# Optimization experiments

Measured on AMD Instinct MI355X. Metric: run time of the kernel, lower is better.

The kernel has to match this reference:

```python
import jax, jax.numpy as jnp
import numpy as np
from jax import lax

RATE = 0.3  # drop_rate from init_kwargs
B, L, E, U, V = 32, 64, 512, 512, 32000


def setup_inputs() -> dict:
    key = jax.random.key(0)
    ks = jax.random.split(key, 9)
    return {
        "pos_embs": jax.random.normal(ks[0], (B, L, E), jnp.float32),
        "images_emb": jax.random.normal(ks[1], (B, E), jnp.float32),
        "targets": jax.random.randint(ks[2], (B, L), 0, V, jnp.int64),
        # learned parameters
        "emb_table": jax.random.normal(ks[3], (V, E), jnp.float32) * 0.02,
        "W_in": jax.random.normal(ks[4], (E, 4 * U), jnp.float32) * 0.05,   # LSTM kernel (gate order i,f,c,o)
        "W_rec": jax.random.normal(ks[5], (U, 4 * U), jnp.float32) * 0.05,  # LSTM recurrent kernel
        "b_lstm": jnp.zeros((4 * U,), jnp.float32),
        "W_out": jax.random.normal(ks[6], (U, V), jnp.float32) * 0.02,
        "b_out": jnp.zeros((V,), jnp.float32),
    }


def _dropout_masks(batch, seq_len):
    """Deterministic dropout masks (training=True in the original)."""
    keep = 1.0 - RATE
    mk = jax.random.key(42)
    k1, k2, k3 = jax.random.split(mk, 3)
    # word dropout: noise_shape=(None,1,E) -> one mask per (batch, feature), shared over time
    word_mask = jax.random.bernoulli(k1, keep, (batch, 1, E)).astype(jnp.float32) / keep
    # Keras recurrent_dropout: 4 masks on h (one per gate), constant across timesteps
    rec_masks = jax.random.bernoulli(k2, keep, (4, batch, U)).astype(jnp.float32) / keep
    # final dropout on rnn_output [B, T, units]
    fin_mask = jax.random.bernoulli(k3, keep, (batch, seq_len, U)).astype(jnp.float32) / keep
    return word_mask, rec_masks, fin_mask


def reference(pos_embs, images_emb, targets, emb_table, W_in, W_rec, b_lstm, W_out, b_out):
    batch = pos_embs.shape[0]
    seq_len = targets.shape[1]  # (L-1) words + 1 image step = L
    word_mask, rec_masks, fin_mask = _dropout_masks(batch, seq_len)

    # embedding + word dropout (mask shared over time axis)
    word_embs = emb_table[targets[:, :-1]] * word_mask            # [B, L-1, E]
    x = jnp.concatenate([images_emb[:, None, :], word_embs], axis=1)  # [B, L, E]

    W_rec_g = W_rec.reshape(U, 4, U)  # [u, gate, u]

    def step(carry, x_t):
        h, c = carry
        z_in = x_t @ W_in + b_lstm                                # [B, 4U]
        # per-gate recurrent dropout on h, then recurrent matmul
        z_rec = jnp.einsum('gbu,ugv->bgv', h[None, :, :] * rec_masks, W_rec_g)
        z = z_in + z_rec.reshape(batch, 4 * U)
        zi, zf, zg, zo = jnp.split(z, 4, axis=-1)
        i = jax.nn.sigmoid(zi)
        f = jax.nn.sigmoid(zf)
        g = jnp.tanh(zg)
        o = jax.nn.sigmoid(zo)
        c_new = f * c + i * g
        h_new = o * jnp.tanh(c_new)
        return (h_new, c_new), h_new

    h0 = jnp.zeros((batch, U), x.dtype)
    (_, _), hs = lax.scan(step, (h0, h0), x.transpose(1, 0, 2))   # hs: [L, B, U]
    rnn_out = hs.transpose(1, 0, 2) * fin_mask                    # [B, L, U]

    predictions = rnn_out @ W_out + b_out                         # [B, L, V]
    return predictions
```

## Files before the change

### kernel.cpp

```cpp
#include <hip/hip_runtime.h>
#include <hip/hip_bf16.h>
#include <cstdint>
#include <cstddef>

struct TF2 { uint32_t a, b; };

__host__ __device__ constexpr uint32_t rotl32(uint32_t v, int r) {
  return (v << r) | (v >> (32 - r));
}

__host__ __device__ constexpr TF2 threefry2x32(uint32_t k0, uint32_t k1,
                                               uint32_t x0, uint32_t x1) {
  uint32_t ks0 = k0, ks1 = k1, ks2 = k0 ^ k1 ^ 0x1BD11BDAu;
  const int rotA[4] = {13, 15, 26, 6};
  const int rotB[4] = {17, 29, 16, 24};
  x0 += ks0; x1 += ks1;
  for (int i = 0; i < 5; ++i) {
    const int* rot = (i % 2 == 0) ? rotA : rotB;
    for (int j = 0; j < 4; ++j) {
      x0 += x1; x1 = rotl32(x1, rot[j]); x1 ^= x0;
    }
    uint32_t ks[3] = {ks0, ks1, ks2};
    x0 += ks[(i + 1) % 3];
    x1 += ks[(i + 2) % 3] + (uint32_t)(i + 1);
  }
  return TF2{x0, x1};
}

__device__ __forceinline__ float jax_mask(uint32_t child, uint32_t idx) {
  TF2 ck = threefry2x32(0u, 42u, 0u, child);
  TF2 r  = threefry2x32(ck.a, ck.b, 0u, idx);
  uint32_t bits = r.a ^ r.b;
  float u = __uint_as_float((bits >> 9) | 0x3f800000u) - 1.0f;
  return (u < 0.7f) ? (1.0f / 0.7f) : 0.0f;
}

__device__ __forceinline__ unsigned short f2bf(float f) {
  uint32_t u = __float_as_uint(f);
  uint32_t r = (u + 0x7fffu + ((u >> 16) & 1u)) >> 16;
  return (unsigned short)r;
}

typedef __attribute__((ext_vector_type(8))) short short8;
typedef __attribute__((ext_vector_type(4))) float f32x4;

__device__ __forceinline__ void async_copy16(const unsigned short* g, unsigned short* l) {
  __builtin_amdgcn_global_load_lds(
      (const __attribute__((address_space(1))) unsigned int*)g,
      (__attribute__((address_space(3))) unsigned int*)l, 16, 0, 0);
}

__global__ __launch_bounds__(256) void build_x_kernel(
    const float* __restrict__ img, const int* __restrict__ tgt,
    const float* __restrict__ emb, unsigned short* __restrict__ x) {
  const int idx = blockIdx.x * 256 + threadIdx.x;
  const int e = idx & 511;
  const int t = (idx >> 9) & 63;
  const int b = idx >> 15;
  float v;
  if (t == 0) {
    v = img[b * 512 + e];
  } else {
    const int w = tgt[b * 64 + (t - 1)];
    const float wm = jax_mask(0u, (uint32_t)(b * 512 + e));
    v = emb[(size_t)w * 512 + e] * wm;
  }
  x[idx] = f2bf(v);
}

__global__ __launch_bounds__(256) void rec_mask_kernel(float* __restrict__ rm) {
  const int idx = blockIdx.x * 256 + threadIdx.x;
  rm[idx] = jax_mask(1u, (uint32_t)idx);
}

__global__ __launch_bounds__(256) void transpose_wrec(
    const float* __restrict__ in, float* __restrict__ out) {
  __shared__ float tile[32][33];
  const int j0 = blockIdx.x * 32;
  const int u0 = blockIdx.y * 32;
  const int tx = threadIdx.x & 31;
  const int ty = threadIdx.x >> 5;
  for (int r = ty; r < 32; r += 8)
    tile[r][tx] = in[(size_t)(u0 + r) * 2048 + (j0 + tx)];
  __syncthreads();
  for (int r = ty; r < 32; r += 8)
    out[(size_t)(j0 + r) * 512 + (u0 + tx)] = tile[tx][r];
}

__global__ __launch_bounds__(256) void transpose_cvt(
    const float* __restrict__ in, unsigned short* __restrict__ out,
    int R, int C) {
  __shared__ float tile[32][33];
  const int c0 = blockIdx.x * 32;
  const int r0 = blockIdx.y * 32;
  const int tx = threadIdx.x & 31;
  const int ty = threadIdx.x >> 5;
  for (int r = ty; r < 32; r += 8)
    tile[r][tx] = in[(size_t)(r0 + r) * C + (c0 + tx)];
  __syncthreads();
  for (int r = ty; r < 32; r += 8)
    out[(size_t)(c0 + r) * R + (r0 + tx)] = f2bf(tile[tx][r]);
}

__global__ __launch_bounds__(256) void gemm_bf16_mfma(
    const unsigned short* __restrict__ A, const unsigned short* __restrict__ BT,
    const float* __restrict__ bias, float* __restrict__ C, int M, int N) {
  __shared__ unsigned short As[128 * 32];
  __shared__ unsigned short Bs[128 * 32];
  const int tid = threadIdx.x;
  const int lane = tid & 63;
  const int wave = tid >> 6;
  const int wm = (wave >> 1) * 64;
  const int wn = (wave & 1) * 64;
  const int m0 = blockIdx.y * 128;
  const int n0 = blockIdx.x * 128;

  f32x4 zero4 = {0.f, 0.f, 0.f, 0.f};
  f32x4 acc[4][4];
#pragma unroll
  for (int i = 0; i < 4; ++i)
#pragma unroll
    for (int j = 0; j < 4; ++j) acc[i][j] = zero4;

  const unsigned short* ga = A + (size_t)(m0 + (tid >> 2)) * 512 + (tid & 3) * 8;
  const unsigned short* gb = BT + (size_t)(n0 + (tid >> 2)) * 512 + (tid & 3) * 8;
  unsigned short* lwA = As + wave * 512;
  unsigned short* lwB = Bs + wave * 512;

  const int fr = lane & 15;
  const int kc = (lane >> 4) * 8;

  for (int k0 = 0; k0 < 512; k0 += 32) {
    __syncthreads();
    async_copy16(ga + k0, lwA);
    async_copy16(ga + k0 + 64 * 512, lwA + 2048);
    async_copy16(gb + k0, lwB);
    async_copy16(gb + k0 + 64 * 512, lwB + 2048);
    __syncthreads();

    short8 af[4], bf[4];
#pragma unroll
    for (int i = 0; i < 4; ++i)
      af[i] = *(const short8*)(As + (wm + i * 16 + fr) * 32 + kc);
#pragma unroll
    for (int i = 0; i < 4; ++i)
      bf[i] = *(const short8*)(Bs + (wn + i * 16 + fr) * 32 + kc);
#pragma unroll
    for (int mi = 0; mi < 4; ++mi)
#pragma unroll
      for (int ni = 0; ni < 4; ++ni)
        acc[mi][ni] = __builtin_amdgcn_mfma_f32_16x16x32_bf16(
            af[mi], bf[ni], acc[mi][ni], 0, 0, 0);
  }

#pragma unroll
  for (int mi = 0; mi < 4; ++mi) {
    const int mrow = m0 + wm + mi * 16 + (lane >> 4) * 4;
#pragma unroll
    for (int ni = 0; ni < 4; ++ni) {
      const int ncol = n0 + wn + ni * 16 + (lane & 15);
      const float bs = bias[ncol];
#pragma unroll
      for (int r2 = 0; r2 < 4; ++r2)
        C[(size_t)(mrow + r2) * N + ncol] = acc[mi][ni][r2] + bs;
    }
  }
}

__global__ __launch_bounds__(256) void lstm_step2(
    const float* __restrict__ zin, const float* __restrict__ WT,
    const float* __restrict__ rm, const float* __restrict__ hmr,
    float* __restrict__ hmw, float* __restrict__ c,
    unsigned short* __restrict__ rnn, const int t) {
  __shared__ __align__(16) float wl[32 * 132];
  __shared__ __align__(16) float hl[32 * 132];
  __shared__ float zsh[4][8][9];
  const int tid = threadIdx.x;
  const int u0 = (blockIdx.x & 63) * 8;
  const int b0 = (blockIdx.x >> 6) * 8;

  const int jl = tid & 31;
  const int bl = tid >> 5;
  const int g = jl >> 3, ul = jl & 7;
  const int b = b0 + bl;
  const float zv = zin[(size_t)(b * 64 + t) * 2048 + g * 512 + u0 + ul];

  const int srow = tid >> 3;
  const int sg = srow >> 3, sr = srow & 7;
  const float* wsrc = WT + (size_t)(sg * 512 + u0 + sr) * 512;
  const float* hsrc = hmr + (size_t)(sg * 32 + b0 + sr) * 512;

  const float4* wp = (const float4*)&wl[jl * 132];
  const float4* hp = (const float4*)&hl[(g * 8 + bl) * 132];

  float4 a0 = {0.f, 0.f, 0.f, 0.f}, a1 = {0.f, 0.f, 0.f, 0.f};

  for (int ph = 0; ph < 4; ++ph) {
    const int kbase = ph * 128;
    __syncthreads();
#pragma unroll
    for (int cc = 0; cc < 4; ++cc) {
      const int ch = (tid & 7) + cc * 8;
      *(float4*)&wl[srow * 132 + ch * 4] = *(const float4*)&wsrc[kbase + ch * 4];
      *(float4*)&hl[srow * 132 + ch * 4] = *(const float4*)&hsrc[kbase + ch * 4];
    }
    __syncthreads();
#pragma unroll 8
    for (int i = 0; i < 32; i += 2) {
      const float4 w0 = wp[i], h0 = hp[i];
      const float4 w1 = wp[i + 1], h1 = hp[i + 1];
      a0.x += w0.x * h0.x; a0.y += w0.y * h0.y;
      a0.z += w0.z * h0.z; a0.w += w0.w * h0.w;
      a1.x += w1.x * h1.x; a1.y += w1.y * h1.y;
      a1.z += w1.z * h1.z; a1.w += w1.w * h1.w;
    }
  }
  const float dot = (a0.x + a0.y + a0.z + a0.w) + (a1.x + a1.y + a1.z + a1.w);
  zsh[g][bl][ul] = zv + dot;
  __syncthreads();

  if (tid < 64) {
    const int uu = tid & 7, bb = tid >> 3;
    const float zi = zsh[0][bb][uu];
    const float zf = zsh[1][bb][uu];
    const float zg = zsh[2][bb][uu];
    const float zo = zsh[3][bb][uu];
    const float i_ = 1.f / (1.f + expf(-zi));
    const float f_ = 1.f / (1.f + expf(-zf));
    const float g_ = tanhf(zg);
    const float o_ = 1.f / (1.f + expf(-zo));
    const int bg = b0 + bb, ug = u0 + uu;
    const size_t cidx = (size_t)bg * 512 + ug;
    const float cn = f_ * c[cidx] + i_ * g_;
    c[cidx] = cn;
    const float hn = o_ * tanhf(cn);
    const float fm = jax_mask(2u, (uint32_t)((bg * 64 + t) * 512 + ug));
    rnn[(size_t)(bg * 64 + t) * 512 + ug] = f2bf(hn * fm);
#pragma unroll
    for (int gg = 0; gg < 4; ++gg) {
      const size_t o = (size_t)(gg * 32 + bg) * 512 + ug;
      hmw[o] = hn * rm[o];
    }
  }
}

extern "C" void kernel_launch(void* const* d_in, const int* in_sizes, int n_in,
                              void* d_out, int out_size, void* d_ws, size_t ws_size,
                              hipStream_t stream) {
  (void)in_sizes; (void)n_in; (void)out_size; (void)ws_size;
  const float* img   = (const float*)d_in[1];
  const int*   tgt   = (const int*)d_in[2];
  const float* emb   = (const float*)d_in[3];
  const float* W_in  = (const float*)d_in[4];
  const float* W_rec = (const float*)d_in[5];
  const float* b_l   = (const float*)d_in[6];
  const float* W_out = (const float*)d_in[7];
  const float* b_o   = (const float*)d_in[8];
  float* out = (float*)d_out;
  float* ws  = (float*)d_ws;

  float* zin = ws;
  float* WT  = ws + 4194304;
  float* hm0 = ws + 5242880;
  float* c   = ws + 5308416;
  float* hm1 = ws + 5324800;
  float* rm  = ws + 5390336;
  unsigned short* us = (unsigned short*)(ws + 5455872);
  unsigned short* x_bf  = us;
  unsigned short* WinT  = us + 1048576;
  unsigned short* rnn   = us + 2097152;
  unsigned short* WoutT = us + 3145728;

  hipMemsetAsync(hm0, 0, (size_t)(65536 + 16384) * sizeof(float), stream);

  build_x_kernel<<<4096, 256, 0, stream>>>(img, tgt, emb, x_bf);
  rec_mask_kernel<<<256, 256, 0, stream>>>(rm);
  transpose_wrec<<<dim3(64, 16), 256, 0, stream>>>(W_rec, WT);
  transpose_cvt<<<dim3(64, 16), 256, 0, stream>>>(W_in, WinT, 512, 2048);
  transpose_cvt<<<dim3(1000, 16), 256, 0, stream>>>(W_out, WoutT, 512, 32000);

  gemm_bf16_mfma<<<dim3(16, 16), 256, 0, stream>>>(x_bf, WinT, b_l, zin, 2048, 2048);

  for (int t = 0; t < 64; ++t) {
    const float* hr = (t & 1) ? hm1 : hm0;
    float*       hw = (t & 1) ? hm0 : hm1;
    lstm_step2<<<256, 256, 0, stream>>>(zin, WT, rm, hr, hw, c, rnn, t);
  }

  gemm_bf16_mfma<<<dim3(250, 16), 256, 0, stream>>>(rnn, WoutT, b_o, out, 2048, 32000);
}
```

Measured before the change: 1.088 ms.

## Replace per-step LSTM launches with persistent kernel using grid barrier and split-bf16 MFMA

Runs the 64 LSTM timesteps inside one persistent 32-block kernel synchronized by an atomic grid barrier, instead of launching one kernel per step. Recurrent weights are kept in registers as hi/lo bf16 pairs and the recurrent matmul uses MFMA with a three-product split to keep near-fp32 accuracy. Recurrent masks and the cell state move into registers. This is meant to remove launch overhead and repeated weight reloads. In exchange it relies on all 32 blocks being co-resident, since the launch is not cooperative, and the split-bf16 products change rounding slightly.

```diff
diff --git a/kernel.cpp b/kernel.cpp
--- a/kernel.cpp
+++ b/kernel.cpp
@@ -39,6 +39,10 @@
   uint32_t u = __float_as_uint(f);
   uint32_t r = (u + 0x7fffu + ((u >> 16) & 1u)) >> 16;
   return (unsigned short)r;
+}
+
+__device__ __forceinline__ float bf2f(unsigned short b) {
+  return __uint_as_float((uint32_t)b << 16);
 }
 
 typedef __attribute__((ext_vector_type(8))) short short8;
@@ -68,11 +72,6 @@
   x[idx] = f2bf(v);
 }
 
-__global__ __launch_bounds__(256) void rec_mask_kernel(float* __restrict__ rm) {
-  const int idx = blockIdx.x * 256 + threadIdx.x;
-  rm[idx] = jax_mask(1u, (uint32_t)idx);
-}
-
 __global__ __launch_bounds__(256) void transpose_wrec(
     const float* __restrict__ in, float* __restrict__ out) {
   __shared__ float tile[32][33];
@@ -167,80 +166,129 @@
   }
 }
 
-__global__ __launch_bounds__(256) void lstm_step2(
+#define HM_PSTRIDE (2 * 4 * 32 * 512)
+#define NBLK 32
+
+__device__ __forceinline__ void grid_barrier(unsigned int* bar, unsigned int target) {
+  __syncthreads();
+  __threadfence();
+  if (threadIdx.x == 0) {
+    __hip_atomic_fetch_add(bar, 1u, __ATOMIC_RELAXED, __HIP_MEMORY_SCOPE_AGENT);
+    while (__hip_atomic_load(bar, __ATOMIC_RELAXED, __HIP_MEMORY_SCOPE_AGENT) < target)
+      __builtin_amdgcn_s_sleep(1);
+  }
+  __syncthreads();
+  __threadfence();
+}
+
+__global__ __launch_bounds__(256, 1) void lstm_coop(
     const float* __restrict__ zin, const float* __restrict__ WT,
-    const float* __restrict__ rm, const float* __restrict__ hmr,
-    float* __restrict__ hmw, float* __restrict__ c,
-    unsigned short* __restrict__ rnn, const int t) {
-  __shared__ __align__(16) float wl[32 * 132];
-  __shared__ __align__(16) float hl[32 * 132];
-  __shared__ float zsh[4][8][9];
+    unsigned short* __restrict__ hm, unsigned short* __restrict__ rnn,
+    unsigned int* __restrict__ bar) {
+  __shared__ float zsh[4][32][17];
   const int tid = threadIdx.x;
-  const int u0 = (blockIdx.x & 63) * 8;
-  const int b0 = (blockIdx.x >> 6) * 8;
-
-  const int jl = tid & 31;
-  const int bl = tid >> 5;
-  const int g = jl >> 3, ul = jl & 7;
-  const int b = b0 + bl;
-  const float zv = zin[(size_t)(b * 64 + t) * 2048 + g * 512 + u0 + ul];
-
-  const int srow = tid >> 3;
-  const int sg = srow >> 3, sr = srow & 7;
-  const float* wsrc = WT + (size_t)(sg * 512 + u0 + sr) * 512;
-  const float* hsrc = hmr + (size_t)(sg * 32 + b0 + sr) * 512;
-
-  const float4* wp = (const float4*)&wl[jl * 132];
-  const float4* hp = (const float4*)&hl[(g * 8 + bl) * 132];
-
-  float4 a0 = {0.f, 0.f, 0.f, 0.f}, a1 = {0.f, 0.f, 0.f, 0.f};
-
-  for (int ph = 0; ph < 4; ++ph) {
-    const int kbase = ph * 128;
+  const int lane = tid & 63;
+  const int g = tid >> 6;
+  const int u0 = blockIdx.x * 16;
+  const int fr = lane & 15;
+  const int kq = (lane >> 4) * 8;
+
+  short8 whi[16], wlo[16];
+  {
+    const float* wrow = WT + (size_t)(g * 512 + u0 + fr) * 512 + kq;
+#pragma unroll
+    for (int kk = 0; kk < 16; ++kk) {
+      const float4 w0 = *(const float4*)(wrow + kk * 32);
+      const float4 w1 = *(const float4*)(wrow + kk * 32 + 4);
+      const float wv[8] = {w0.x, w0.y, w0.z, w0.w, w1.x, w1.y, w1.z, w1.w};
+      short8 h8, l8;
+#pragma unroll
+      for (int e = 0; e < 8; ++e) {
+        const unsigned short hb = f2bf(wv[e]);
+        h8[e] = (short)hb;
+        l8[e] = (short)f2bf(wv[e] - bf2f(hb));
+      }
+      whi[kk] = h8; wlo[kk] = l8;
+    }
+  }
+
+  const int ab = tid >> 4;
+  const int uc = tid & 15;
+  const int au = u0 + uc;
+  float rmask[2][4];
+#pragma unroll
+  for (int cc = 0; cc < 2; ++cc)
+#pragma unroll
+    for (int gg = 0; gg < 4; ++gg)
+      rmask[cc][gg] = jax_mask(1u, (uint32_t)((gg * 32 + ab + cc * 16) * 512 + au));
+  float c0 = 0.f, c1 = 0.f;
+
+  for (int t = 0; t < 64; ++t) {
+    const int rp = t & 1;
+    f32x4 ahh0 = {0,0,0,0}, ahl0 = {0,0,0,0}, alh0 = {0,0,0,0};
+    f32x4 ahh1 = {0,0,0,0}, ahl1 = {0,0,0,0}, alh1 = {0,0,0,0};
+
+    if (t) {
+      const unsigned short* hb  = hm + (size_t)rp * HM_PSTRIDE;
+      const unsigned short* hhi = hb + (size_t)((0 * 4 + g) * 32) * 512;
+      const unsigned short* hlo = hb + (size_t)((1 * 4 + g) * 32) * 512;
+#pragma unroll
+      for (int kk = 0; kk < 16; ++kk) {
+        const int ko = kk * 32 + kq;
+        const short8 ah0 = *(const short8*)(hhi + (size_t)(fr) * 512 + ko);
+        const short8 ah1 = *(const short8*)(hhi + (size_t)(16 + fr) * 512 + ko);
+        const short8 al0 = *(const short8*)(hlo + (size_t)(fr) * 512 + ko);
+        const short8 al1 = *(const short8*)(hlo + (size_t)(16 + fr) * 512 + ko);
+        ahh0 = __builtin_amdgcn_mfma_f32_16x16x32_bf16(ah0, whi[kk], ahh0, 0, 0, 0);
+        ahh1 = __builtin_amdgcn_mfma_f32_16x16x32_bf16(ah1, whi[kk], ahh1, 0, 0, 0);
+        ahl0 = __builtin_amdgcn_mfma_f32_16x16x32_bf16(ah0, wlo[kk], ahl0, 0, 0, 0);
+        ahl1 = __builtin_amdgcn_mfma_f32_16x16x32_bf16(ah1, wlo[kk], ahl1, 0, 0, 0);
+        alh0 = __builtin_amdgcn_mfma_f32_16x16x32_bf16(al0, whi[kk], alh0, 0, 0, 0);
+        alh1 = __builtin_amdgcn_mfma_f32_16x16x32_bf16(al1, whi[kk], alh1, 0, 0, 0);
+      }
+    }
+
+#pragma unroll
+    for (int r = 0; r < 4; ++r) {
+      zsh[g][(lane >> 4) * 4 + r][fr]      = ahh0[r] + ahl0[r] + alh0[r];
+      zsh[g][16 + (lane >> 4) * 4 + r][fr] = ahh1[r] + ahl1[r] + alh1[r];
+    }
     __syncthreads();
-#pragma unroll
-    for (int cc = 0; cc < 4; ++cc) {
-      const int ch = (tid & 7) + cc * 8;
-      *(float4*)&wl[srow * 132 + ch * 4] = *(const float4*)&wsrc[kbase + ch * 4];
-      *(float4*)&hl[srow * 132 + ch * 4] = *(const float4*)&hsrc[kbase + ch * 4];
-    }
-    __syncthreads();
-#pragma unroll 8
-    for (int i = 0; i < 32; i += 2) {
-      const float4 w0 = wp[i], h0 = hp[i];
-      const float4 w1 = wp[i + 1], h1 = hp[i + 1];
-      a0.x += w0.x * h0.x; a0.y += w0.y * h0.y;
-      a0.z += w0.z * h0.z; a0.w += w0.w * h0.w;
-      a1.x += w1.x * h1.x; a1.y += w1.y * h1.y;
-      a1.z += w1.z * h1.z; a1.w += w1.w * h1.w;
-    }
-  }
-  const float dot = (a0.x + a0.y + a0.z + a0.w) + (a1.x + a1.y + a1.z + a1.w);
-  zsh[g][bl][ul] = zv + dot;
-  __syncthreads();
-
-  if (tid < 64) {
-    const int uu = tid & 7, bb = tid >> 3;
-    const float zi = zsh[0][bb][uu];
-    const float zf = zsh[1][bb][uu];
-    const float zg = zsh[2][bb][uu];
-    const float zo = zsh[3][bb][uu];
-    const float i_ = 1.f / (1.f + expf(-zi));
-    const float f_ = 1.f / (1.f + expf(-zf));
-    const float g_ = tanhf(zg);
-    const float o_ = 1.f / (1.f + expf(-zo));
-    const int bg = b0 + bb, ug = u0 + uu;
-    const size_t cidx = (size_t)bg * 512 + ug;
-    const float cn = f_ * c[cidx] + i_ * g_;
-    c[cidx] = cn;
-    const float hn = o_ * tanhf(cn);
-    const float fm = jax_mask(2u, (uint32_t)((bg * 64 + t) * 512 + ug));
-    rnn[(size_t)(bg * 64 + t) * 512 + ug] = f2bf(hn * fm);
-#pragma unroll
-    for (int gg = 0; gg < 4; ++gg) {
-      const size_t o = (size_t)(gg * 32 + bg) * 512 + ug;
-      hmw[o] = hn * rm[o];
-    }
+
+    float hn[2];
+#pragma unroll
+    for (int cc = 0; cc < 2; ++cc) {
+      const int b = ab + cc * 16;
+      const size_t zo = (size_t)(b * 64 + t) * 2048 + au;
+      const float zi = zsh[0][b][uc] + zin[zo];
+      const float zf = zsh[1][b][uc] + zin[zo + 512];
+      const float zg = zsh[2][b][uc] + zin[zo + 1024];
+      const float zz = zsh[3][b][uc] + zin[zo + 1536];
+      const float i_ = 1.f / (1.f + expf(-zi));
+      const float f_ = 1.f / (1.f + expf(-zf));
+      const float g_ = tanhf(zg);
+      const float o_ = 1.f / (1.f + expf(-zz));
+      float& c = cc ? c1 : c0;
+      c = f_ * c + i_ * g_;
+      hn[cc] = o_ * tanhf(c);
+      const float fm = jax_mask(2u, (uint32_t)((b * 64 + t) * 512 + au));
+      rnn[(size_t)(b * 64 + t) * 512 + au] = f2bf(hn[cc] * fm);
+    }
+
+    unsigned short* hw = hm + (size_t)(rp ^ 1) * HM_PSTRIDE;
+#pragma unroll
+    for (int cc = 0; cc < 2; ++cc) {
+      const int b = ab + cc * 16;
+#pragma unroll
+      for (int gg = 0; gg < 4; ++gg) {
+        const float v = hn[cc] * rmask[cc][gg];
+        const unsigned short hb = f2bf(v);
+        hw[(size_t)((0 * 4 + gg) * 32 + b) * 512 + au] = hb;
+        hw[(size_t)((1 * 4 + gg) * 32 + b) * 512 + au] = f2bf(v - bf2f(hb));
+      }
+    }
+
+    grid_barrier(bar, (unsigned int)(NBLK * (t + 1)));
   }
 }
 
@@ -261,31 +309,24 @@
 
   float* zin = ws;
   float* WT  = ws + 4194304;
-  float* hm0 = ws + 5242880;
-  float* c   = ws + 5308416;
-  float* hm1 = ws + 5324800;
-  float* rm  = ws + 5390336;
+  unsigned short* hm = (unsigned short*)(ws + 5242880);
+  unsigned int* bar  = (unsigned int*)(ws + 5440000);
   unsigned short* us = (unsigned short*)(ws + 5455872);
   unsigned short* x_bf  = us;
   unsigned short* WinT  = us + 1048576;
   unsigned short* rnn   = us + 2097152;
   unsigned short* WoutT = us + 3145728;
 
-  hipMemsetAsync(hm0, 0, (size_t)(65536 + 16384) * sizeof(float), stream);
+  hipMemsetAsync(bar, 0, 64, stream);
 
   build_x_kernel<<<4096, 256, 0, stream>>>(img, tgt, emb, x_bf);
-  rec_mask_kernel<<<256, 256, 0, stream>>>(rm);
   transpose_wrec<<<dim3(64, 16), 256, 0, stream>>>(W_rec, WT);
   transpose_cvt<<<dim3(64, 16), 256, 0, stream>>>(W_in, WinT, 512, 2048);
   transpose_cvt<<<dim3(1000, 16), 256, 0, stream>>>(W_out, WoutT, 512, 32000);
 
   gemm_bf16_mfma<<<dim3(16, 16), 256, 0, stream>>>(x_bf, WinT, b_l, zin, 2048, 2048);
 
-  for (int t = 0; t < 64; ++t) {
-    const float* hr = (t & 1) ? hm1 : hm0;
-    float*       hw = (t & 1) ? hm0 : hm1;
-    lstm_step2<<<256, 256, 0, stream>>>(zin, WT, rm, hr, hw, c, rnn, t);
-  }
+  lstm_coop<<<32, 256, 0, stream>>>(zin, WT, hm, rnn, bar);
 
   gemm_bf16_mfma<<<dim3(250, 16), 256, 0, stream>>>(rnn, WoutT, b_o, out, 2048, 32000);
 }
```

Result: slower. 1.438 ms (+32.2%).

## Run LSTM recurrent matmul on MFMA with split-bf16 hi/lo precision

Applied to the files above, without the earlier changes.

The per-step recurrent matmul moves from scalar FP32 FMA over LDS tiles to bf16 MFMA instructions. To keep near-FP32 accuracy, both W_rec and the masked hidden state are split into bf16 hi and lo parts, and three MFMAs (hh, hl, lh) are accumulated per k-slice. Operands are read directly from global memory without LDS staging. K is split across two wave groups, and the grid changes to 64 blocks of 512 threads with 16x16 tiles. This cuts per-step compute latency but uses fewer blocks, triples MFMA work, and adds a small precision risk from the split representation.

```diff
diff --git a/kernel.cpp b/kernel.cpp
--- a/kernel.cpp
+++ b/kernel.cpp
@@ -41,6 +41,10 @@
   return (unsigned short)r;
 }
 
+__device__ __forceinline__ float bf2f(unsigned short b) {
+  return __uint_as_float((uint32_t)b << 16);
+}
+
 typedef __attribute__((ext_vector_type(8))) short short8;
 typedef __attribute__((ext_vector_type(4))) float f32x4;
 
@@ -73,8 +77,9 @@
   rm[idx] = jax_mask(1u, (uint32_t)idx);
 }
 
-__global__ __launch_bounds__(256) void transpose_wrec(
-    const float* __restrict__ in, float* __restrict__ out) {
+__global__ __launch_bounds__(256) void transpose_wrec_hilo(
+    const float* __restrict__ in, unsigned short* __restrict__ hi,
+    unsigned short* __restrict__ lo) {
   __shared__ float tile[32][33];
   const int j0 = blockIdx.x * 32;
   const int u0 = blockIdx.y * 32;
@@ -83,8 +88,12 @@
   for (int r = ty; r < 32; r += 8)
     tile[r][tx] = in[(size_t)(u0 + r) * 2048 + (j0 + tx)];
   __syncthreads();
-  for (int r = ty; r < 32; r += 8)
-    out[(size_t)(j0 + r) * 512 + (u0 + tx)] = tile[tx][r];
+  for (int r = ty; r < 32; r += 8) {
+    const float v = tile[tx][r];
+    const unsigned short hb = f2bf(v);
+    hi[(size_t)(j0 + r) * 512 + (u0 + tx)] = hb;
+    lo[(size_t)(j0 + r) * 512 + (u0 + tx)] = f2bf(v - bf2f(hb));
+  }
 }
 
 __global__ __launch_bounds__(256) void transpose_cvt(
@@ -167,79 +176,73 @@
   }
 }
 
-__global__ __launch_bounds__(256) void lstm_step2(
-    const float* __restrict__ zin, const float* __restrict__ WT,
-    const float* __restrict__ rm, const float* __restrict__ hmr,
-    float* __restrict__ hmw, float* __restrict__ c,
+__global__ __launch_bounds__(512) void lstm_step3(
+    const float* __restrict__ zin, const unsigned short* __restrict__ whi,
+    const unsigned short* __restrict__ wlo, const float* __restrict__ rm,
+    unsigned short* __restrict__ am, float* __restrict__ c,
     unsigned short* __restrict__ rnn, const int t) {
-  __shared__ __align__(16) float wl[32 * 132];
-  __shared__ __align__(16) float hl[32 * 132];
-  __shared__ float zsh[4][8][9];
+  __shared__ float zsh[2][4][16][17];
   const int tid = threadIdx.x;
-  const int u0 = (blockIdx.x & 63) * 8;
-  const int b0 = (blockIdx.x >> 6) * 8;
-
-  const int jl = tid & 31;
-  const int bl = tid >> 5;
-  const int g = jl >> 3, ul = jl & 7;
-  const int b = b0 + bl;
-  const float zv = zin[(size_t)(b * 64 + t) * 2048 + g * 512 + u0 + ul];
-
-  const int srow = tid >> 3;
-  const int sg = srow >> 3, sr = srow & 7;
-  const float* wsrc = WT + (size_t)(sg * 512 + u0 + sr) * 512;
-  const float* hsrc = hmr + (size_t)(sg * 32 + b0 + sr) * 512;
-
-  const float4* wp = (const float4*)&wl[jl * 132];
-  const float4* hp = (const float4*)&hl[(g * 8 + bl) * 132];
-
-  float4 a0 = {0.f, 0.f, 0.f, 0.f}, a1 = {0.f, 0.f, 0.f, 0.f};
-
-  for (int ph = 0; ph < 4; ++ph) {
-    const int kbase = ph * 128;
-    __syncthreads();
-#pragma unroll
-    for (int cc = 0; cc < 4; ++cc) {
-      const int ch = (tid & 7) + cc * 8;
-      *(float4*)&wl[srow * 132 + ch * 4] = *(const float4*)&wsrc[kbase + ch * 4];
-      *(float4*)&hl[srow * 132 + ch * 4] = *(const float4*)&hsrc[kbase + ch * 4];
-    }
-    __syncthreads();
-#pragma unroll 8
-    for (int i = 0; i < 32; i += 2) {
-      const float4 w0 = wp[i], h0 = hp[i];
-      const float4 w1 = wp[i + 1], h1 = hp[i + 1];
-      a0.x += w0.x * h0.x; a0.y += w0.y * h0.y;
-      a0.z += w0.z * h0.z; a0.w += w0.w * h0.w;
-      a1.x += w1.x * h1.x; a1.y += w1.y * h1.y;
-      a1.z += w1.z * h1.z; a1.w += w1.w * h1.w;
-    }
-  }
-  const float dot = (a0.x + a0.y + a0.z + a0.w) + (a1.x + a1.y + a1.z + a1.w);
-  zsh[g][bl][ul] = zv + dot;
+  const int lane = tid & 63;
+  const int wv = tid >> 6;
+  const int g = wv & 3;
+  const int kh = wv >> 2;
+  const int u0 = blockIdx.x * 16;
+  const int b0 = blockIdx.y * 16;
+  const int fr = lane & 15;
+  const int kq = (lane >> 4) * 8;
+  const int rp = t & 1;
+
+  f32x4 ahh = {0,0,0,0}, ahl = {0,0,0,0}, alh = {0,0,0,0};
+
+  const unsigned short* abase = am + (size_t)rp * 131072
+      + (size_t)g * 32768 + (size_t)(b0 + fr) * 512 + kh * 256 + kq;
+  const size_t woff = (size_t)(g * 512 + u0 + fr) * 512 + kh * 256 + kq;
+  const unsigned short* wh = whi + woff;
+  const unsigned short* wl = wlo + woff;
+
+#pragma unroll
+  for (int j = 0; j < 8; ++j) {
+    const short8 ah = *(const short8*)(abase + j * 32);
+    const short8 al = *(const short8*)(abase + 16384 + j * 32);
+    const short8 w0 = *(const short8*)(wh + j * 32);
+    const short8 w1 = *(const short8*)(wl + j * 32);
+    ahh = __builtin_amdgcn_mfma_f32_16x16x32_bf16(ah, w0, ahh, 0, 0, 0);
+    ahl = __builtin_amdgcn_mfma_f32_16x16x32_bf16(ah, w1, ahl, 0, 0, 0);
+    alh = __builtin_amdgcn_mfma_f32_16x16x32_bf16(al, w0, alh, 0, 0, 0);
+  }
+
+#pragma unroll
+  for (int r = 0; r < 4; ++r)
+    zsh[kh][g][(lane >> 4) * 4 + r][fr] = ahh[r] + ahl[r] + alh[r];
   __syncthreads();
 
-  if (tid < 64) {
-    const int uu = tid & 7, bb = tid >> 3;
-    const float zi = zsh[0][bb][uu];
-    const float zf = zsh[1][bb][uu];
-    const float zg = zsh[2][bb][uu];
-    const float zo = zsh[3][bb][uu];
+  if (tid < 256) {
+    const int bl = tid >> 4, ul = tid & 15;
+    const int b = b0 + bl, u = u0 + ul;
+    const size_t zo = (size_t)(b * 64 + t) * 2048 + u;
+    const float zi = zsh[0][0][bl][ul] + zsh[1][0][bl][ul] + zin[zo];
+    const float zf = zsh[0][1][bl][ul] + zsh[1][1][bl][ul] + zin[zo + 512];
+    const float zg = zsh[0][2][bl][ul] + zsh[1][2][bl][ul] + zin[zo + 1024];
+    const float zz = zsh[0][3][bl][ul] + zsh[1][3][bl][ul] + zin[zo + 1536];
     const float i_ = 1.f / (1.f + expf(-zi));
     const float f_ = 1.f / (1.f + expf(-zf));
     const float g_ = tanhf(zg);
-    const float o_ = 1.f / (1.f + expf(-zo));
-    const int bg = b0 + bb, ug = u0 + uu;
-    const size_t cidx = (size_t)bg * 512 + ug;
+    const float o_ = 1.f / (1.f + expf(-zz));
+    const size_t cidx = (size_t)b * 512 + u;
     const float cn = f_ * c[cidx] + i_ * g_;
     c[cidx] = cn;
     const float hn = o_ * tanhf(cn);
-    const float fm = jax_mask(2u, (uint32_t)((bg * 64 + t) * 512 + ug));
-    rnn[(size_t)(bg * 64 + t) * 512 + ug] = f2bf(hn * fm);
+    const float fm = jax_mask(2u, (uint32_t)((b * 64 + t) * 512 + u));
+    rnn[(size_t)(b * 64 + t) * 512 + u] = f2bf(hn * fm);
+
+    unsigned short* aw = am + (size_t)(rp ^ 1) * 131072;
 #pragma unroll
     for (int gg = 0; gg < 4; ++gg) {
-      const size_t o = (size_t)(gg * 32 + bg) * 512 + ug;
-      hmw[o] = hn * rm[o];
+      const float v = hn * rm[(size_t)(gg * 32 + b) * 512 + u];
+      const unsigned short hb = f2bf(v);
+      aw[(size_t)gg * 32768 + (size_t)b * 512 + u] = hb;
+      aw[(size_t)gg * 32768 + 16384 + (size_t)b * 512 + u] = f2bf(v - bf2f(hb));
     }
   }
 }
@@ -260,32 +263,30 @@
   float* ws  = (float*)d_ws;
 
   float* zin = ws;
-  float* WT  = ws + 4194304;
-  float* hm0 = ws + 5242880;
-  float* c   = ws + 5308416;
-  float* hm1 = ws + 5324800;
-  float* rm  = ws + 5390336;
-  unsigned short* us = (unsigned short*)(ws + 5455872);
-  unsigned short* x_bf  = us;
-  unsigned short* WinT  = us + 1048576;
-  unsigned short* rnn   = us + 2097152;
-  unsigned short* WoutT = us + 3145728;
-
-  hipMemsetAsync(hm0, 0, (size_t)(65536 + 16384) * sizeof(float), stream);
+  float* rm  = ws + 4194304;
+  float* c   = ws + 4259840;
+  unsigned short* us = (unsigned short*)(ws + 4276224);
+  unsigned short* am    = us;
+  unsigned short* whi   = us + 262144;
+  unsigned short* wlo   = us + 1310720;
+  unsigned short* x_bf  = us + 2359296;
+  unsigned short* WinT  = us + 3407872;
+  unsigned short* rnn   = us + 4456448;
+  unsigned short* WoutT = us + 5505024;
+
+  hipMemsetAsync(am, 0, 262144 * sizeof(unsigned short), stream);
+  hipMemsetAsync(c, 0, 16384 * sizeof(float), stream);
 
   build_x_kernel<<<4096, 256, 0, stream>>>(img, tgt, emb, x_bf);
   rec_mask_kernel<<<256, 256, 0, stream>>>(rm);
-  transpose_wrec<<<dim3(64, 16), 256, 0, stream>>>(W_rec, WT);
+  transpose_wrec_hilo<<<dim3(64, 16), 256, 0, stream>>>(W_rec, whi, wlo);
   transpose_cvt<<<dim3(64, 16), 256, 0, stream>>>(W_in, WinT, 512, 2048);
   transpose_cvt<<<dim3(1000, 16), 256, 0, stream>>>(W_out, WoutT, 512, 32000);
 
   gemm_bf16_mfma<<<dim3(16, 16), 256, 0, stream>>>(x_bf, WinT, b_l, zin, 2048, 2048);
 
-  for (int t = 0; t < 64; ++t) {
-    const float* hr = (t & 1) ? hm1 : hm0;
-    float*       hw = (t & 1) ? hm0 : hm1;
-    lstm_step2<<<256, 256, 0, stream>>>(zin, WT, rm, hr, hw, c, rnn, t);
-  }
+  for (int t = 0; t < 64; ++t)
+    lstm_step3<<<dim3(32, 2), 512, 0, stream>>>(zin, whi, wlo, rm, am, c, rnn, t);
 
   gemm_bf16_mfma<<<dim3(250, 16), 256, 0, stream>>>(rnn, WoutT, b_o, out, 2048, 32000);
 }
```

After: 1.149 ms. 1.06x slower.
